# Performance work log

Measured on AMD Instinct MI355X. Metric: run time of the kernel, lower is better.

## Reference

```python
import jax, jax.numpy as jnp
import numpy as np

EMBED_DIM = 1024
N_HEADS = 16
HEAD_DIM = EMBED_DIM // N_HEADS

def setup_inputs() -> dict:
    key = jax.random.key(0)
    kx, kq, kk, kv, ko = jax.random.split(key, 5)
    s = 1.0 / np.sqrt(EMBED_DIM)
    return {
        "x": jax.random.normal(kx, (4, 2048, EMBED_DIM), dtype=jnp.float32),
        "Wq": jax.random.normal(kq, (EMBED_DIM, EMBED_DIM), dtype=jnp.float32) * s,
        "Wk": jax.random.normal(kk, (EMBED_DIM, EMBED_DIM), dtype=jnp.float32) * s,
        "Wv": jax.random.normal(kv, (EMBED_DIM, EMBED_DIM), dtype=jnp.float32) * s,
        "Wo": jax.random.normal(ko, (EMBED_DIM, EMBED_DIM), dtype=jnp.float32) * s,
    }

def reference(x, Wq, Wk, Wv, Wo):
    B, T, D = x.shape
    H, Dh = N_HEADS, HEAD_DIM
    # projections (nn.Linear: y = x @ W.T); split heads -> [B, H, T, Dh]
    Q = (x @ Wq.T).reshape(B, T, H, Dh).transpose(0, 2, 1, 3)
    K = (x @ Wk.T).reshape(B, T, H, Dh).transpose(0, 2, 1, 3)
    V = (x @ Wv.T).reshape(B, T, H, Dh).transpose(0, 2, 1, 3)
    scores = jnp.einsum("bhqd,bhkd->bhqk", Q, K) / jnp.sqrt(jnp.float32(Dh))
    attn = jax.nn.softmax(scores, axis=-1)
    out = jnp.einsum("bhqk,bhkd->bhqd", attn, V)  # [B,H,T,Dh]
    out = out.transpose(0, 2, 1, 3).reshape(B, T, D)
    return out @ Wo.T
```

## Files before the change

### kernel.cpp

```cpp
#include <hip/hip_runtime.h>

typedef _Float16 f16;
typedef _Float16 f16x8 __attribute__((ext_vector_type(8)));
typedef _Float16 f16x4 __attribute__((ext_vector_type(4)));
typedef float f32x4 __attribute__((ext_vector_type(4)));

#define MFMA16(a, b, c) __builtin_amdgcn_mfma_f32_16x16x32_f16((a), (b), (c), 0, 0, 0)
#define MEMBAR() __asm__ __volatile__("" ::: "memory")

__device__ __forceinline__ void cp16(const f16* g, f16* l) {
  __builtin_amdgcn_global_load_lds(
      (const __attribute__((address_space(1))) void*)g,
      (__attribute__((address_space(3))) void*)l, 16, 0, 0);
}

__global__ __launch_bounds__(256) void cvt_all(
    const float* __restrict__ x,  const float* __restrict__ Wq,
    const float* __restrict__ Wk, const float* __restrict__ Wv,
    const float* __restrict__ Wo,
    f16* __restrict__ X16, f16* __restrict__ Wq16, f16* __restrict__ Wk16,
    f16* __restrict__ Wv16, f16* __restrict__ Wo16) {
  int blk = blockIdx.x;
  const float* src; f16* dst; size_t off;
  if (blk < 4096) { src = x; dst = X16; off = (size_t)blk * 2048; }
  else {
    int t = blk - 4096, widx = t >> 9, loc = t & 511;
    src = (widx == 0) ? Wq : (widx == 1) ? Wk : (widx == 2) ? Wv : Wo;
    dst = (widx == 0) ? Wq16 : (widx == 1) ? Wk16 : (widx == 2) ? Wv16 : Wo16;
    off = (size_t)loc * 2048;
  }
  size_t e = off + (size_t)threadIdx.x * 8;
  const float4* s = (const float4*)(src + e);
  float4 a = s[0], b = s[1];
  f16x8 o;
  o[0] = (f16)a.x; o[1] = (f16)a.y; o[2] = (f16)a.z; o[3] = (f16)a.w;
  o[4] = (f16)b.x; o[5] = (f16)b.y; o[6] = (f16)b.z; o[7] = (f16)b.w;
  *(f16x8*)(dst + e) = o;
}

__device__ __forceinline__ void gemm_core(
    const f16* __restrict__ A, const f16* __restrict__ B, void* __restrict__ Cv,
    bool outF16, bool permT, int N, int K, int bm, int bn, float scale,
    f16* As, f16* Bs) {
  const int tid = threadIdx.x;
  const int lane = tid & 63, w = tid >> 6;
  const int wm = w >> 1, wn = w & 1;
  const int c = lane & 15, q = lane >> 4;
  const int key = (c >> 1) & 3;
  f32x4 acc[4][4] = {};

  const int Lrow = lane >> 2, Lp = (lane & 3) ^ ((lane >> 3) & 3);
  auto stage = [&](int k0, int bufi) {
#pragma unroll
    for (int j = 0; j < 2; ++j) {
      int r0 = (w * 2 + j) * 16;
      cp16(A + (size_t)(bm + r0 + Lrow) * K + k0 + Lp * 8,
           As + bufi * 4096 + r0 * 32 + lane * 8);
    }
#pragma unroll
    for (int j = 0; j < 2; ++j) {
      int r0 = (w * 2 + j) * 16;
      cp16(B + (size_t)(bn + r0 + Lrow) * K + k0 + Lp * 8,
           Bs + bufi * 4096 + r0 * 32 + lane * 8);
    }
  };

  stage(0, 0);
  const int NIT = K >> 5;
  for (int i = 0; i < NIT; ++i) {
    if (i + 1 < NIT) {
      stage((i + 1) << 5, (i + 1) & 1);
      __builtin_amdgcn_s_waitcnt(0x0F74);
    } else {
      __builtin_amdgcn_s_waitcnt(0x0F70);
    }
    __builtin_amdgcn_s_barrier();
    MEMBAR();
    const f16* Ab = As + (i & 1) * 4096;
    const f16* Bb = Bs + (i & 1) * 4096;
    f16x8 af[4], bf[4];
#pragma unroll
    for (int mt = 0; mt < 4; ++mt)
      af[mt] = *(const f16x8*)(Ab + (wm * 64 + mt * 16 + c) * 32 + (q ^ key) * 8);
#pragma unroll
    for (int nt = 0; nt < 4; ++nt)
      bf[nt] = *(const f16x8*)(Bb + (wn * 64 + nt * 16 + c) * 32 + (q ^ key) * 8);
#pragma unroll
    for (int mt = 0; mt < 4; ++mt)
#pragma unroll
      for (int nt = 0; nt < 4; ++nt)
        acc[mt][nt] = MFMA16(af[mt], bf[nt], acc[mt][nt]);
    MEMBAR();
    __builtin_amdgcn_s_barrier();
  }

#pragma unroll
  for (int mt = 0; mt < 4; ++mt)
#pragma unroll
    for (int nt = 0; nt < 4; ++nt)
#pragma unroll
      for (int r = 0; r < 4; ++r) {
        size_t row = bm + wm * 64 + mt * 16 + q * 4 + r;
        size_t col = bn + wn * 64 + nt * 16 + c;
        if (permT) {
          int t = (int)col & 63;
          col = (col & ~(size_t)63) |
                (size_t)((t & 0x23) | ((t & 0x0C) << 1) | ((t & 0x10) >> 2));
        }
        float v = acc[mt][nt][r] * scale;
        if (outF16) ((f16*)Cv)[row * N + col] = (f16)v;
        else ((float*)Cv)[row * N + col] = v;
      }
}

__global__ __launch_bounds__(256, 4) void gemm_qkvt(
    const f16* __restrict__ X, const f16* __restrict__ Wq,
    const f16* __restrict__ Wk, const f16* __restrict__ Wv,
    f16* __restrict__ Q, f16* __restrict__ Ko, f16* __restrict__ VT, float cs) {
  __shared__ __align__(16) f16 As[8192], Bs[8192];
  const int z = blockIdx.z, x = blockIdx.x;
  if (z < 2) {
    gemm_core(X, z ? Wk : Wq, z ? (void*)Ko : (void*)Q, true, false, 1024, 1024,
              (x >> 3) * 128, (x & 7) * 128, z ? 1.0f : cs, As, Bs);
  } else {
    gemm_core(Wv, X, (void*)VT, true, true, 8192, 1024,
              (x >> 6) * 128, (x & 63) * 128, 1.0f, As, Bs);
  }
}

__global__ __launch_bounds__(256, 4) void gemm_o(
    const f16* __restrict__ A, const f16* __restrict__ Wo, float* __restrict__ out) {
  __shared__ __align__(16) f16 As[8192], Bs[8192];
  const int x = blockIdx.x;
  gemm_core(A, Wo, (void*)out, false, false, 1024, 1024,
            (x >> 3) * 128, (x & 7) * 128, 1.0f, As, Bs);
}

__global__ __launch_bounds__(256, 2) void attn_kernel(
    const f16* __restrict__ Qg, const f16* __restrict__ Kg,
    const f16* __restrict__ VTg, f16* __restrict__ Og) {
  const int T = 2048, D = 1024;
  const int x = blockIdx.x;
  const int xcd = x & 7, rem = x >> 3;
  const int qt = rem & 7, grp = rem >> 3;
  const int bh = (grp << 3) | xcd;
  const int b = bh >> 4, h = bh & 15;
  const size_t base = ((size_t)b * T) * D + h * 64;
  const size_t baseV = (size_t)h * 64 * 8192 + (size_t)b * T;
  __shared__ __align__(16) f16 smem[16384];
  const int tid = threadIdx.x;
  const int lane = tid & 63, w = tid >> 6;
  const int c = lane & 15, q = lane >> 4;
  const int cx = c & 7;
  f16* Kb = smem;
  f16* Vb = smem + 8192;

#pragma unroll
  for (int j = 0; j < 8; ++j) {
    int cb = (w * 8 + j) * 64;
    int ch = cb + lane;
    int row = ch >> 3, p = (ch & 7) ^ (row & 7);
    cp16(Qg + base + (size_t)(qt * 256 + row) * D + p * 8, smem + cb * 8);
  }
  __syncthreads();
  f16x8 qf[4][2];
#pragma unroll
  for (int g = 0; g < 4; ++g)
#pragma unroll
    for (int kh = 0; kh < 2; ++kh)
      qf[g][kh] = *(const f16x8*)(smem + (w * 64 + g * 16 + c) * 64 + ((kh * 4 + q) ^ cx) * 8);
  __syncthreads();

  float l_[4] = {0.f, 0.f, 0.f, 0.f};
  f32x4 o_[4][4] = {};

  auto stageKV = [&](int kv, int bufi) {
    f16* Ks = Kb + bufi * 4096;
    f16* Vt = Vb + bufi * 4096;
#pragma unroll
    for (int j = 0; j < 2; ++j) {
      int cb = (w * 2 + j) * 64;
      int ch = cb + lane;
      int row = ch >> 3, p = (ch & 7) ^ (row & 7);
      cp16(Kg + base + (size_t)(kv + row) * D + p * 8, Ks + cb * 8);
    }
#pragma unroll
    for (int j = 0; j < 2; ++j) {
      int cb = (w * 2 + j) * 64;
      int ch = cb + lane;
      int row = ch >> 3, p = (ch & 7) ^ (row & 7);
      cp16(VTg + baseV + (size_t)row * 8192 + kv + p * 8, Vt + cb * 8);
    }
  };

  stageKV(0, 0);
  for (int i = 0; i < 32; ++i) {
    if (i < 31) {
      stageKV((i + 1) * 64, (i + 1) & 1);
      __builtin_amdgcn_s_waitcnt(0x0F74);
    } else {
      __builtin_amdgcn_s_waitcnt(0x0F70);
    }
    __builtin_amdgcn_s_barrier();

    f16* Ks = Kb + (i & 1) * 4096;
    f16* Vt = Vb + (i & 1) * 4096;

#pragma unroll
    for (int hk = 0; hk < 2; ++hk) {
      f32x4 st[2][4] = {};
#pragma unroll
      for (int kh = 0; kh < 2; ++kh) {
        f16x8 kf[2];
#pragma unroll
        for (int mt = 0; mt < 2; ++mt)
          kf[mt] = *(const f16x8*)(Ks + ((hk * 2 + mt) * 16 + c) * 64 + ((kh * 4 + q) ^ cx) * 8);
        __builtin_amdgcn_s_setprio(1);
#pragma unroll
        for (int mt = 0; mt < 2; ++mt)
#pragma unroll
          for (int g = 0; g < 4; ++g)
            st[mt][g] = MFMA16(kf[mt], qf[g][kh], st[mt][g]);
        __builtin_amdgcn_s_setprio(0);
      }

      f16x8 pf[4];
#pragma unroll
      for (int g = 0; g < 4; ++g) {
        float s = 0.f;
#pragma unroll
        for (int mt = 0; mt < 2; ++mt) {
          float p0 = __builtin_amdgcn_exp2f(st[mt][g][0]);
          float p1 = __builtin_amdgcn_exp2f(st[mt][g][1]);
          float p2 = __builtin_amdgcn_exp2f(st[mt][g][2]);
          float p3 = __builtin_amdgcn_exp2f(st[mt][g][3]);
          s += (p0 + p1) + (p2 + p3);
          int hh = mt * 4;
          pf[g][hh + 0] = (f16)p0; pf[g][hh + 1] = (f16)p1;
          pf[g][hh + 2] = (f16)p2; pf[g][hh + 3] = (f16)p3;
        }
        l_[g] += s;
      }

      __builtin_amdgcn_s_setprio(1);
#pragma unroll
      for (int d = 0; d < 4; ++d) {
        f16x8 vf = *(const f16x8*)(Vt + (d * 16 + c) * 64 + ((hk * 4 + q) ^ cx) * 8);
        o_[0][d] = MFMA16(pf[0], vf, o_[0][d]);
        o_[1][d] = MFMA16(pf[1], vf, o_[1][d]);
        o_[2][d] = MFMA16(pf[2], vf, o_[2][d]);
        o_[3][d] = MFMA16(pf[3], vf, o_[3][d]);
      }
      __builtin_amdgcn_s_setprio(0);
    }
    MEMBAR();
    __builtin_amdgcn_s_barrier();
  }

#pragma unroll
  for (int g = 0; g < 4; ++g) {
    l_[g] += __shfl_xor(l_[g], 16);
    l_[g] += __shfl_xor(l_[g], 32);
  }

#pragma unroll
  for (int g = 0; g < 4; ++g)
#pragma unroll
    for (int r = 0; r < 4; ++r) {
      float linv = 1.0f / __shfl(l_[g], q * 4 + r);
      size_t row = (size_t)qt * 256 + w * 64 + g * 16 + q * 4 + r;
#pragma unroll
      for (int d = 0; d < 4; ++d)
        Og[base + row * D + d * 16 + c] = (f16)(o_[g][d][r] * linv);
    }
}

extern "C" void kernel_launch(void* const* d_in, const int* in_sizes, int n_in,
                              void* d_out, int out_size, void* d_ws, size_t ws_size,
                              hipStream_t stream) {
  const float* x  = (const float*)d_in[0];
  const float* Wq = (const float*)d_in[1];
  const float* Wk = (const float*)d_in[2];
  const float* Wv = (const float*)d_in[3];
  const float* Wo = (const float*)d_in[4];
  char* ws = (char*)d_ws;
  const size_t MB = 1ull << 20;
  f16* X16  = (f16*)(ws + 0 * MB);
  f16* Wq16 = (f16*)(ws + 16 * MB);
  f16* Wk16 = (f16*)(ws + 18 * MB);
  f16* Wv16 = (f16*)(ws + 20 * MB);
  f16* Wo16 = (f16*)(ws + 22 * MB);
  f16* Q16  = (f16*)(ws + 24 * MB);
  f16* K16  = (f16*)(ws + 40 * MB);
  f16* VT16 = (f16*)(ws + 56 * MB);
  f16* A16  = (f16*)(ws + 72 * MB);

  const float cs = 0.18033688011112042f;

  cvt_all<<<6144, 256, 0, stream>>>(x, Wq, Wk, Wv, Wo,
                                    X16, Wq16, Wk16, Wv16, Wo16);

  gemm_qkvt<<<dim3(512, 1, 3), 256, 0, stream>>>(
      X16, Wq16, Wk16, Wv16, Q16, K16, VT16, cs);

  attn_kernel<<<dim3(512, 1, 1), 256, 0, stream>>>(Q16, K16, VT16, A16);

  gemm_o<<<512, 256, 0, stream>>>(A16, Wo16, (float*)d_out);
}
```

Measured before the change: 259.6 us.

## Triple-buffer K/V tiles in attention and drop trailing per-iteration barrier

Moves the attention kernel's K/V staging from double to triple buffering. Tiles are prefetched two iterations ahead, and the end-of-iteration barrier is removed, leaving one barrier per iteration. The inner loop now computes all 64 keys of scores at once rather than in two halves. This hides more global-load latency and cuts synchronization, at the cost of more LDS (48KB per block, which may limit occupancy at 2 blocks per CU) and more live score registers.

```diff
diff --git a/kernel.cpp b/kernel.cpp
--- a/kernel.cpp
+++ b/kernel.cpp
@@ -147,13 +147,13 @@
   const int b = bh >> 4, h = bh & 15;
   const size_t base = ((size_t)b * T) * D + h * 64;
   const size_t baseV = (size_t)h * 64 * 8192 + (size_t)b * T;
-  __shared__ __align__(16) f16 smem[16384];
+  __shared__ __align__(16) f16 smem[24576];
   const int tid = threadIdx.x;
   const int lane = tid & 63, w = tid >> 6;
   const int c = lane & 15, q = lane >> 4;
   const int cx = c & 7;
   f16* Kb = smem;
-  f16* Vb = smem + 8192;
+  f16* Vb = smem + 12288;
 
 #pragma unroll
   for (int j = 0; j < 8; ++j) {
@@ -194,67 +194,64 @@
   };
 
   stageKV(0, 0);
+  stageKV(64, 1);
   for (int i = 0; i < 32; ++i) {
-    if (i < 31) {
-      stageKV((i + 1) * 64, (i + 1) & 1);
-      __builtin_amdgcn_s_waitcnt(0x0F74);
-    } else {
-      __builtin_amdgcn_s_waitcnt(0x0F70);
-    }
+    if (i < 31) __builtin_amdgcn_s_waitcnt(0x0F74);
+    else        __builtin_amdgcn_s_waitcnt(0x0F70);
     __builtin_amdgcn_s_barrier();
-
-    f16* Ks = Kb + (i & 1) * 4096;
-    f16* Vt = Vb + (i & 1) * 4096;
-
-#pragma unroll
-    for (int hk = 0; hk < 2; ++hk) {
-      f32x4 st[2][4] = {};
-#pragma unroll
-      for (int kh = 0; kh < 2; ++kh) {
-        f16x8 kf[2];
-#pragma unroll
-        for (int mt = 0; mt < 2; ++mt)
-          kf[mt] = *(const f16x8*)(Ks + ((hk * 2 + mt) * 16 + c) * 64 + ((kh * 4 + q) ^ cx) * 8);
-        __builtin_amdgcn_s_setprio(1);
-#pragma unroll
-        for (int mt = 0; mt < 2; ++mt)
-#pragma unroll
-          for (int g = 0; g < 4; ++g)
-            st[mt][g] = MFMA16(kf[mt], qf[g][kh], st[mt][g]);
-        __builtin_amdgcn_s_setprio(0);
+    MEMBAR();
+    if (i + 2 < 32) stageKV((i + 2) * 64, (i + 2) % 3);
+
+    const f16* Ks = Kb + (i % 3) * 4096;
+    const f16* Vt = Vb + (i % 3) * 4096;
+
+    f32x4 st[4][4] = {};
+#pragma unroll
+    for (int kh = 0; kh < 2; ++kh) {
+      f16x8 kf[4];
+#pragma unroll
+      for (int mt = 0; mt < 4; ++mt)
+        kf[mt] = *(const f16x8*)(Ks + (mt * 16 + c) * 64 + ((kh * 4 + q) ^ cx) * 8);
+      __builtin_amdgcn_s_setprio(1);
+#pragma unroll
+      for (int mt = 0; mt < 4; ++mt)
+#pragma unroll
+        for (int g = 0; g < 4; ++g)
+          st[mt][g] = MFMA16(kf[mt], qf[g][kh], st[mt][g]);
+      __builtin_amdgcn_s_setprio(0);
+    }
+
+    f16x8 pf[4][2];
+#pragma unroll
+    for (int g = 0; g < 4; ++g) {
+      float s = 0.f;
+#pragma unroll
+      for (int mt = 0; mt < 4; ++mt) {
+        float p0 = __builtin_amdgcn_exp2f(st[mt][g][0]);
+        float p1 = __builtin_amdgcn_exp2f(st[mt][g][1]);
+        float p2 = __builtin_amdgcn_exp2f(st[mt][g][2]);
+        float p3 = __builtin_amdgcn_exp2f(st[mt][g][3]);
+        s += (p0 + p1) + (p2 + p3);
+        int kc = mt >> 1, hh = (mt & 1) * 4;
+        pf[g][kc][hh + 0] = (f16)p0; pf[g][kc][hh + 1] = (f16)p1;
+        pf[g][kc][hh + 2] = (f16)p2; pf[g][kc][hh + 3] = (f16)p3;
       }
-
-      f16x8 pf[4];
-#pragma unroll
-      for (int g = 0; g < 4; ++g) {
-        float s = 0.f;
-#pragma unroll
-        for (int mt = 0; mt < 2; ++mt) {
-          float p0 = __builtin_amdgcn_exp2f(st[mt][g][0]);
-          float p1 = __builtin_amdgcn_exp2f(st[mt][g][1]);
-          float p2 = __builtin_amdgcn_exp2f(st[mt][g][2]);
-          float p3 = __builtin_amdgcn_exp2f(st[mt][g][3]);
-          s += (p0 + p1) + (p2 + p3);
-          int hh = mt * 4;
-          pf[g][hh + 0] = (f16)p0; pf[g][hh + 1] = (f16)p1;
-          pf[g][hh + 2] = (f16)p2; pf[g][hh + 3] = (f16)p3;
-        }
-        l_[g] += s;
+      l_[g] += s;
+    }
+
+    __builtin_amdgcn_s_setprio(1);
+#pragma unroll
+    for (int kc = 0; kc < 2; ++kc)
+#pragma unroll
+      for (int d = 0; d < 4; ++d) {
+        f16x8 vf = *(const f16x8*)(Vt + (d * 16 + c) * 64 + ((kc * 4 + q) ^ cx) * 8);
+        o_[0][d] = MFMA16(pf[0][kc], vf, o_[0][d]);
+        o_[1][d] = MFMA16(pf[1][kc], vf, o_[1][d]);
+        o_[2][d] = MFMA16(pf[2][kc], vf, o_[2][d]);
+        o_[3][d] = MFMA16(pf[3][kc], vf, o_[3][d]);
       }
-
-      __builtin_amdgcn_s_setprio(1);
-#pragma unroll
-      for (int d = 0; d < 4; ++d) {
-        f16x8 vf = *(const f16x8*)(Vt + (d * 16 + c) * 64 + ((hk * 4 + q) ^ cx) * 8);
-        o_[0][d] = MFMA16(pf[0], vf, o_[0][d]);
-        o_[1][d] = MFMA16(pf[1], vf, o_[1][d]);
-        o_[2][d] = MFMA16(pf[2], vf, o_[2][d]);
-        o_[3][d] = MFMA16(pf[3], vf, o_[3][d]);
-      }
-      __builtin_amdgcn_s_setprio(0);
-    }
+    __builtin_amdgcn_s_setprio(0);
     MEMBAR();
-    __builtin_amdgcn_s_barrier();
   }
 
 #pragma unroll
```

Result: no change. 254.6 us (-1.9%).
